# Kernel tuning notes

Hardware: AMD Instinct MI355X
Metric: run time of the kernel (lower is better)

Reference implementation:

```python
import jax, jax.numpy as jnp
import numpy as np

B, IN, OUT = 2048, 64, 2048


def setup_inputs() -> dict:
    key = jax.random.key(0)
    k1, k2, k3 = jax.random.split(key, 3)
    x = jax.random.normal(k1, (B, IN), dtype=jnp.float32)
    # learned params (shapes per init: means [in, out], inv_std_dev [out, in, in])
    means = jax.random.uniform(k2, (IN, OUT), dtype=jnp.float32)
    # roughly like the inverse of a diagonal step matrix plus small noise
    inv_std_dev = (jax.random.normal(k3, (OUT, IN, IN), dtype=jnp.float32) * 0.05
                   + jnp.eye(IN, dtype=jnp.float32) * 0.5)
    return {"x": x, "means": means, "inv_std_dev": inv_std_dev}


def reference(x, means, inv_std_dev):
    # diff[b, o, i] = x[b, i] - means[i, o]   -> [B, OUT, IN]
    d = x[:, None, :] - means.T[None, :, :]
    # torch uses inv_std_dev.pow(2) (elementwise square), not a matrix square
    A = inv_std_dev * inv_std_dev  # [OUT, IN, IN]
    # per-neuron quadratic form: q[b, o] = d[b,o,:] @ A[o] @ d[b,o,:]
    q = jnp.einsum('boi,oij,boj->bo', d, A, d)
    return jnp.exp(-0.5 * q)  # [B, OUT]
```

## Files before the change

### kernel.cpp

```cpp
#include <hip/hip_runtime.h>
#include <hip/hip_bf16.h>

typedef __bf16 bf16x8 __attribute__((ext_vector_type(8)));
typedef float f32x16 __attribute__((ext_vector_type(16)));

#define B_N 2048
#define O_N 2048
#define K_TRI 2080
#define K_TOT 2304
#define K_STEPS 36

__device__ __forceinline__ void gld16(const void* g, void* l) {
    __builtin_amdgcn_global_load_lds(
        (const __attribute__((address_space(1))) void*)g,
        (__attribute__((address_space(3))) void*)l,
        16, 0, 0);
}

__global__ __launch_bounds__(256) void rbf_prepA(
    const float* __restrict__ inv, const float* __restrict__ means,
    const float* __restrict__ x, __bf16* __restrict__ Srm,
    __bf16* __restrict__ Pt)
{
    __shared__ float s[64 * 65];
    __shared__ float mld[64];
    __shared__ float uw[128];
    __shared__ unsigned short ptab[K_TRI];

    const int t = threadIdx.x;
    {
        int base = 0;
#pragma unroll 1
        for (int i = 0; i < 64; ++i) {
            if (t < 64 - i) ptab[base + t] = (unsigned short)((i << 8) | (i + t));
            base += 64 - i;
        }
    }

    if ((int)blockIdx.x < O_N) {
        const int o = blockIdx.x;
        const float4* src = (const float4*)(inv + (size_t)o * 4096);
#pragma unroll
        for (int k = 0; k < 4; ++k) {
            const int idx = k * 256 + t;
            const float4 v = src[idx];
            const int i = idx >> 4;
            const int j0 = (idx & 15) * 4;
            s[i * 65 + j0 + 0] = v.x * v.x;
            s[i * 65 + j0 + 1] = v.y * v.y;
            s[i * 65 + j0 + 2] = v.z * v.z;
            s[i * 65 + j0 + 3] = v.w * v.w;
        }
        if (t < 64) mld[t] = means[(size_t)t * O_N + o];
        __syncthreads();
        if (t < 64) {
            float u = 0.f;
#pragma unroll
            for (int i = 0; i < 64; ++i) u = fmaf(s[i * 65 + t], mld[i], u);
            uw[t] = u;
        } else if (t < 128) {
            const int j = t - 64;
            float w = 0.f;
#pragma unroll
            for (int i = 0; i < 64; ++i) w = fmaf(s[j * 65 + i], mld[i], w);
            uw[64 + j] = w;
        }
        __syncthreads();
        __bf16* Srow = Srm + (size_t)o * K_TOT;
#pragma unroll 1
        for (int c = t; c < K_TOT; c += 256) {
            float v;
            if (c < K_TRI) {
                const int ij = ptab[c];
                const int i = ij >> 8, j = ij & 255;
                v = (i == j) ? s[i * 65 + i] : (s[i * 65 + j] + s[j * 65 + i]);
            } else if (c < 2272) {
                const int j = (c - K_TRI) & 63;
                const float cv = -(uw[j] + uw[64 + j]);
                const __bf16 hi = (__bf16)cv;
                v = (c < 2208) ? (float)hi : (cv - (float)hi);
            } else if (c < 2274) {
                float kk = 0.f;
#pragma unroll
                for (int j = 0; j < 64; ++j) kk = fmaf(uw[j], mld[j], kk);
                const __bf16 khi = (__bf16)kk;
                v = (c == 2272) ? (float)khi : (kk - (float)khi);
            } else v = 0.f;
            Srow[c] = (__bf16)v;
        }
    } else {
        const int b0r = ((int)blockIdx.x - O_N) * 8;
#pragma unroll
        for (int q = 0; q < 2; ++q) {
            const int idx = q * 256 + t;
            s[(idx >> 6) * 65 + (idx & 63)] =
                x[(size_t)(b0r + (idx >> 6)) * 64 + (idx & 63)];
        }
        __syncthreads();
#pragma unroll 1
        for (int q = 0; q < 9; ++q) {
            const int task = q * 256 + t;
            const int c8 = task >> 3, r8 = task & 7;
            const float* xr = &s[r8 * 65];
            unsigned short w8[8];
#pragma unroll
            for (int e = 0; e < 8; ++e) {
                const int c = c8 * 8 + e;
                float v;
                if (c < K_TRI) {
                    const int ij = ptab[c];
                    v = xr[ij >> 8] * xr[ij & 255];
                } else if (c < 2272) {
                    const float xv = xr[(c - K_TRI) & 63];
                    const __bf16 hi = (__bf16)xv;
                    v = (c < 2144) ? (float)hi
                      : (c < 2208) ? (xv - (float)hi) : (float)hi;
                } else if (c < 2274) v = 1.f;
                else v = 0.f;
                w8[e] = __builtin_bit_cast(unsigned short, (__bf16)v);
            }
            *(bf16x8*)(Pt + ((size_t)c8 * 2048 + b0r + r8) * 8) =
                *(const bf16x8*)w8;
        }
    }
}

__global__ __launch_bounds__(256, 2) void rbf_prepB(
    const __bf16* __restrict__ Srm, __bf16* __restrict__ St)
{
    __shared__ __align__(16) char ts[64 * 1156];
    const int t = threadIdx.x;
    const int tb = (int)blockIdx.x >> 2;
    const int cp = (int)blockIdx.x & 3;
    const int o0 = tb * 64;

#pragma unroll 1
    for (int q = 0; q < 18; ++q) {
        const int idx = q * 256 + t;
        const int r = idx / 72, c = idx % 72;
        const float4 v = *(const float4*)((const char*)Srm
                          + (size_t)(o0 + r) * (K_TOT * 2) + cp * 1152 + c * 16);
        *(float4*)(&ts[r * 1156 + c * 16]) = v;
    }
    __syncthreads();
#pragma unroll 1
    for (int q = 0; q < 18; ++q) {
        const int idx = q * 256 + t;
        const int c = idx >> 6, r = idx & 63;
        const float4 v = *(const float4*)(&ts[r * 1156 + c * 16]);
        *(float4*)((char*)St + ((size_t)(cp * 72 + c) * 2048 + o0 + r) * 16) = v;
    }
}

__global__ __launch_bounds__(256, 2) void rbf_gemm(
    const __bf16* __restrict__ P, const __bf16* __restrict__ S,
    float* __restrict__ out)
{
    __shared__ __align__(16) char sAB[3][24576];

    const int tid = threadIdx.x;
    const int lane = tid & 63;
    const int w = tid >> 6;
    const int wr = w >> 1, wc = w & 1;
    const int cl = lane & 31;
    const int h = lane >> 5;

    const int wg = (int)blockIdx.x;
    const int xcd = wg & 7;
    const int loc = wg >> 3;
    const int oBase = (xcd * 4 + (loc & 3)) * 64;
    const int bBase = (loc >> 2) * 128;

    const char* gsrc[6];
    int ldst[6];
#pragma unroll
    for (int r = 0; r < 6; ++r) {
        if (r < 4) {
            const int ks = 2 * r + (tid >> 7);
            const int row = tid & 127;
            ldst[r] = r * 4096 + tid * 16;
            gsrc[r] = (const char*)P + ((size_t)ks * 2048 + bBase + row) * 16;
        } else {
            const int ks = (r - 4) * 4 + (tid >> 6);
            const int row = tid & 63;
            ldst[r] = 16384 + (r - 4) * 4096 + tid * 16;
            gsrc[r] = (const char*)S + ((size_t)ks * 2048 + oBase + row) * 16;
        }
    }

#define RBF_STAGE(ST) do {                                                    \
    const size_t goA_ = (size_t)(ST) * 262144;       \
    const size_t goB_ = (size_t)(ST) * 262144;    \
    char* d_ = &sAB[(ST) % 3][0];                                             \
    _Pragma("unroll")                                                         \
    for (int r_ = 0; r_ < 4; ++r_) gld16(gsrc[r_] + goA_, d_ + ldst[r_]);     \
    _Pragma("unroll")                                                         \
    for (int r_ = 4; r_ < 6; ++r_) gld16(gsrc[r_] + goB_, d_ + ldst[r_]);     \
} while (0)

    RBF_STAGE(0);
    RBF_STAGE(1);

    const f32x16 zz = {0.f,0.f,0.f,0.f,0.f,0.f,0.f,0.f,
                       0.f,0.f,0.f,0.f,0.f,0.f,0.f,0.f};
    f32x16 acc0 = zz, acc1 = zz;

    const int aoff = (wr * 64 + cl) * 16;
    const int boff = 16384 + (wc * 32 + cl) * 16;

#pragma unroll 1
    for (int st = 0; st < K_STEPS; ++st) {
        __builtin_amdgcn_s_barrier();
        if (st + 2 < K_STEPS) {
            RBF_STAGE(st + 2);
            asm volatile("s_waitcnt vmcnt(12)" ::: "memory");
        } else if (st + 1 < K_STEPS) {
            asm volatile("s_waitcnt vmcnt(6)" ::: "memory");
        } else {
            asm volatile("s_waitcnt vmcnt(0)" ::: "memory");
        }
        __builtin_amdgcn_s_barrier();
        __builtin_amdgcn_sched_barrier(0);
        const char* bp = &sAB[st % 3][0];

        __builtin_amdgcn_s_setprio(1);
#pragma unroll
        for (int sl = 0; sl < 4; ++sl) {
            const int ks = sl * 2 + h;
            const bf16x8 a0 = *(const bf16x8*)(bp + ks * 2048 + aoff);
            const bf16x8 a1 = *(const bf16x8*)(bp + ks * 2048 + aoff + 512);
            const bf16x8 b0 = *(const bf16x8*)(bp + ks * 1024 + boff);
            acc0 = __builtin_amdgcn_mfma_f32_32x32x16_bf16(a0, b0, acc0, 0, 0, 0);
            acc1 = __builtin_amdgcn_mfma_f32_32x32x16_bf16(a1, b0, acc1, 0, 0, 0);
        }
        __builtin_amdgcn_s_setprio(0);
    }
#undef RBF_STAGE

#pragma unroll
    for (int r = 0; r < 16; ++r) {
        const int row32 = (r & 3) + 8 * (r >> 2) + 4 * h;
        const int col = oBase + wc * 32 + cl;
        out[(size_t)(bBase + wr * 64 + row32) * O_N + col] =
            exp2f(acc0[r] * -0.72134752044448170368f);
        out[(size_t)(bBase + wr * 64 + 32 + row32) * O_N + col] =
            exp2f(acc1[r] * -0.72134752044448170368f);
    }
}

extern "C" void kernel_launch(void* const* d_in, const int* in_sizes, int n_in,
                              void* d_out, int out_size, void* d_ws, size_t ws_size,
                              hipStream_t stream)
{
    const float* x = (const float*)d_in[0];
    const float* means = (const float*)d_in[1];
    const float* inv = (const float*)d_in[2];
    float* out = (float*)d_out;

    const size_t SZ = (size_t)O_N * K_TOT * sizeof(__bf16);
    __bf16* St  = (__bf16*)d_ws;
    __bf16* Pt  = (__bf16*)((char*)d_ws + SZ);
    __bf16* Srm = (__bf16*)((char*)d_ws + 2 * SZ);

    rbf_prepA<<<dim3(O_N + 256), dim3(256), 0, stream>>>(inv, means, x, Srm, Pt);
    rbf_prepB<<<dim3(128), dim3(256), 0, stream>>>(Srm, St);
    rbf_gemm<<<dim3(512), dim3(256), 0, stream>>>(Pt, St, out);

    (void)in_sizes; (void)n_in; (void)out_size; (void)ws_size;
}
```

Before: 65.69 us.

## Split GEMM K dimension in two with 128x128 tiles and separate exp reduce

Enlarges the GEMM block tile from 64x128 to 128x128, with four accumulators per wave, and splits the K range into two halves. This keeps 512 blocks while raising MFMA work per LDS load. Each half writes fp32 partial sums to workspace, and a new reduce kernel adds the two halves and applies the exponential. The LDS ring grows to four buffers, which lets the loop drop one barrier per step. The cost is writing and re-reading two full fp32 output-sized partial buffers plus an extra kernel launch.

```diff
diff --git a/kernel.cpp b/kernel.cpp
--- a/kernel.cpp
+++ b/kernel.cpp
@@ -2,6 +2,7 @@
 #include <hip/hip_bf16.h>
 
 typedef __bf16 bf16x8 __attribute__((ext_vector_type(8)));
+typedef float f32x4 __attribute__((ext_vector_type(4)));
 typedef float f32x16 __attribute__((ext_vector_type(16)));
 
 #define B_N 2048
@@ -9,6 +10,7 @@
 #define K_TRI 2080
 #define K_TOT 2304
 #define K_STEPS 36
+#define STEP_B 131072
 
 __device__ __forceinline__ void gld16(const void* g, void* l) {
     __builtin_amdgcn_global_load_lds(
@@ -152,11 +154,11 @@
     }
 }
 
-__global__ __launch_bounds__(256, 2) void rbf_gemm(
+__global__ __launch_bounds__(256, 2) void rbf_gemm_sk(
     const __bf16* __restrict__ P, const __bf16* __restrict__ S,
-    float* __restrict__ out)
-{
-    __shared__ __align__(16) char sAB[3][24576];
+    float* __restrict__ Cpart)
+{
+    __shared__ __align__(16) char sAB[4][16384];
 
     const int tid = threadIdx.x;
     const int lane = tid & 63;
@@ -168,34 +170,30 @@
     const int wg = (int)blockIdx.x;
     const int xcd = wg & 7;
     const int loc = wg >> 3;
-    const int oBase = (xcd * 4 + (loc & 3)) * 64;
-    const int bBase = (loc >> 2) * 128;
-
-    const char* gsrc[6];
-    int ldst[6];
-#pragma unroll
-    for (int r = 0; r < 6; ++r) {
-        if (r < 4) {
-            const int ks = 2 * r + (tid >> 7);
-            const int row = tid & 127;
-            ldst[r] = r * 4096 + tid * 16;
-            gsrc[r] = (const char*)P + ((size_t)ks * 2048 + bBase + row) * 16;
-        } else {
-            const int ks = (r - 4) * 4 + (tid >> 6);
-            const int row = tid & 63;
-            ldst[r] = 16384 + (r - 4) * 4096 + tid * 16;
-            gsrc[r] = (const char*)S + ((size_t)ks * 2048 + oBase + row) * 16;
-        }
+    const int kh = loc & 1;
+    const int opan = (loc >> 1) & 1;
+    const int bpan = loc >> 2;
+    const int oBase = (xcd * 2 + opan) * 128;
+    const int bBase = bpan * 128;
+    const int kc = kh * 144;
+
+    const char* gsrc[4];
+#pragma unroll
+    for (int q = 0; q < 4; ++q) {
+        const int ks = (q & 1) * 2 + (tid >> 7);
+        const int row = tid & 127;
+        gsrc[q] = (q < 2)
+            ? (const char*)P + ((size_t)(kc + ks) * 2048 + bBase + row) * 16
+            : (const char*)S + ((size_t)(kc + ks) * 2048 + oBase + row) * 16;
     }
 
 #define RBF_STAGE(ST) do {                                                    \
-    const size_t goA_ = (size_t)(ST) * 262144;       \
-    const size_t goB_ = (size_t)(ST) * 262144;    \
-    char* d_ = &sAB[(ST) % 3][0];                                             \
-    _Pragma("unroll")                                                         \
-    for (int r_ = 0; r_ < 4; ++r_) gld16(gsrc[r_] + goA_, d_ + ldst[r_]);     \
-    _Pragma("unroll")                                                         \
-    for (int r_ = 4; r_ < 6; ++r_) gld16(gsrc[r_] + goB_, d_ + ldst[r_]);     \
+    const size_t go_ = (size_t)(ST) * STEP_B;                                 \
+    char* d_ = &sAB[(ST) & 3][0];                                             \
+    gld16(gsrc[0] + go_, d_ + 0    + tid * 16);                               \
+    gld16(gsrc[1] + go_, d_ + 4096 + tid * 16);                               \
+    gld16(gsrc[2] + go_, d_ + 8192  + tid * 16);                              \
+    gld16(gsrc[3] + go_, d_ + 12288 + tid * 16);                              \
 } while (0)
 
     RBF_STAGE(0);
@@ -203,48 +201,72 @@
 
     const f32x16 zz = {0.f,0.f,0.f,0.f,0.f,0.f,0.f,0.f,
                        0.f,0.f,0.f,0.f,0.f,0.f,0.f,0.f};
-    f32x16 acc0 = zz, acc1 = zz;
+    f32x16 acc00 = zz, acc01 = zz, acc10 = zz, acc11 = zz;
 
     const int aoff = (wr * 64 + cl) * 16;
-    const int boff = 16384 + (wc * 32 + cl) * 16;
+    const int boff = 8192 + (wc * 64 + cl) * 16;
 
 #pragma unroll 1
     for (int st = 0; st < K_STEPS; ++st) {
-        __builtin_amdgcn_s_barrier();
         if (st + 2 < K_STEPS) {
             RBF_STAGE(st + 2);
-            asm volatile("s_waitcnt vmcnt(12)" ::: "memory");
+            asm volatile("s_waitcnt vmcnt(8)" ::: "memory");
         } else if (st + 1 < K_STEPS) {
-            asm volatile("s_waitcnt vmcnt(6)" ::: "memory");
+            asm volatile("s_waitcnt vmcnt(4)" ::: "memory");
         } else {
             asm volatile("s_waitcnt vmcnt(0)" ::: "memory");
         }
         __builtin_amdgcn_s_barrier();
         __builtin_amdgcn_sched_barrier(0);
-        const char* bp = &sAB[st % 3][0];
+        const char* bp = &sAB[st & 3][0];
 
         __builtin_amdgcn_s_setprio(1);
 #pragma unroll
-        for (int sl = 0; sl < 4; ++sl) {
-            const int ks = sl * 2 + h;
-            const bf16x8 a0 = *(const bf16x8*)(bp + ks * 2048 + aoff);
-            const bf16x8 a1 = *(const bf16x8*)(bp + ks * 2048 + aoff + 512);
-            const bf16x8 b0 = *(const bf16x8*)(bp + ks * 1024 + boff);
-            acc0 = __builtin_amdgcn_mfma_f32_32x32x16_bf16(a0, b0, acc0, 0, 0, 0);
-            acc1 = __builtin_amdgcn_mfma_f32_32x32x16_bf16(a1, b0, acc1, 0, 0, 0);
+        for (int s = 0; s < 2; ++s) {
+            const int kso = (s * 2 + h) * 2048;
+            const bf16x8 a0 = *(const bf16x8*)(bp + kso + aoff);
+            const bf16x8 a1 = *(const bf16x8*)(bp + kso + aoff + 512);
+            const bf16x8 b0 = *(const bf16x8*)(bp + kso + boff);
+            const bf16x8 b1 = *(const bf16x8*)(bp + kso + boff + 512);
+            acc00 = __builtin_amdgcn_mfma_f32_32x32x16_bf16(a0, b0, acc00, 0, 0, 0);
+            acc01 = __builtin_amdgcn_mfma_f32_32x32x16_bf16(a0, b1, acc01, 0, 0, 0);
+            acc10 = __builtin_amdgcn_mfma_f32_32x32x16_bf16(a1, b0, acc10, 0, 0, 0);
+            acc11 = __builtin_amdgcn_mfma_f32_32x32x16_bf16(a1, b1, acc11, 0, 0, 0);
         }
         __builtin_amdgcn_s_setprio(0);
     }
 #undef RBF_STAGE
 
+    float* Cp = Cpart + (size_t)kh * O_N * B_N;
 #pragma unroll
     for (int r = 0; r < 16; ++r) {
         const int row32 = (r & 3) + 8 * (r >> 2) + 4 * h;
-        const int col = oBase + wc * 32 + cl;
-        out[(size_t)(bBase + wr * 64 + row32) * O_N + col] =
-            exp2f(acc0[r] * -0.72134752044448170368f);
-        out[(size_t)(bBase + wr * 64 + 32 + row32) * O_N + col] =
-            exp2f(acc1[r] * -0.72134752044448170368f);
+        const size_t r0 = (size_t)(bBase + wr * 64 + row32) * O_N;
+        const size_t r1 = (size_t)(bBase + wr * 64 + 32 + row32) * O_N;
+        const int c0 = oBase + wc * 64 + cl;
+        const int c1 = oBase + wc * 64 + 32 + cl;
+        Cp[r0 + c0] = acc00[r];
+        Cp[r0 + c1] = acc01[r];
+        Cp[r1 + c0] = acc10[r];
+        Cp[r1 + c1] = acc11[r];
+    }
+}
+
+__global__ __launch_bounds__(256) void rbf_reduce(
+    const float* __restrict__ C0, const float* __restrict__ C1,
+    float* __restrict__ out)
+{
+    const size_t base = ((size_t)blockIdx.x * 256 + threadIdx.x) * 8;
+#pragma unroll
+    for (int q = 0; q < 2; ++q) {
+        const size_t i = base + q * 4;
+        const f32x4 a = *(const f32x4*)(C0 + i);
+        const f32x4 b = *(const f32x4*)(C1 + i);
+        f32x4 r;
+#pragma unroll
+        for (int e = 0; e < 4; ++e)
+            r[e] = exp2f((a[e] + b[e]) * -0.72134752044448170368f);
+        *(f32x4*)(out + i) = r;
     }
 }
 
@@ -258,13 +280,17 @@
     float* out = (float*)d_out;
 
     const size_t SZ = (size_t)O_N * K_TOT * sizeof(__bf16);
+    const size_t CZ = (size_t)O_N * B_N * sizeof(float);
     __bf16* St  = (__bf16*)d_ws;
     __bf16* Pt  = (__bf16*)((char*)d_ws + SZ);
     __bf16* Srm = (__bf16*)((char*)d_ws + 2 * SZ);
+    float*  C0  = (float*)((char*)d_ws + 3 * SZ);
+    float*  C1  = (float*)((char*)d_ws + 3 * SZ + CZ);
 
     rbf_prepA<<<dim3(O_N + 256), dim3(256), 0, stream>>>(inv, means, x, Srm, Pt);
     rbf_prepB<<<dim3(128), dim3(256), 0, stream>>>(Srm, St);
-    rbf_gemm<<<dim3(512), dim3(256), 0, stream>>>(Pt, St, out);
+    rbf_gemm_sk<<<dim3(512), dim3(256), 0, stream>>>(Pt, St, C0);
+    rbf_reduce<<<dim3(2048), dim3(256), 0, stream>>>(C0, C1, out);
 
     (void)in_sizes; (void)n_in; (void)out_size; (void)ws_size;
 }
```

After: 70.02 us. +6.6%, slower.
